# Performance work log

Measured on AMD Instinct MI355X. Metric: run time of the kernel, lower is better.

Reference implementation:

```python
import jax, jax.numpy as jnp
import numpy as np

EMBED_DIM = 1024
NUM_HEADS = 16
HEAD_DIM = EMBED_DIM // NUM_HEADS


def setup_inputs() -> dict:
    key = jax.random.key(0)
    ks = jax.random.split(key, 10)
    s = 1.0 / np.sqrt(EMBED_DIM)
    inp = {
        "x1": jax.random.normal(ks[0], (4, 1024, EMBED_DIM), jnp.float32),
        "x2": jax.random.normal(ks[1], (4, 2048, EMBED_DIM), jnp.float32),
        "Wq": jax.random.normal(ks[2], (EMBED_DIM, EMBED_DIM), jnp.float32) * s,
        "bq": jnp.zeros((EMBED_DIM,), jnp.float32),
        "Wk": jax.random.normal(ks[3], (EMBED_DIM, EMBED_DIM), jnp.float32) * s,
        "bk": jnp.zeros((EMBED_DIM,), jnp.float32),
        "Wv": jax.random.normal(ks[4], (EMBED_DIM, EMBED_DIM), jnp.float32) * s,
        "bv": jnp.zeros((EMBED_DIM,), jnp.float32),
        "Wo": jax.random.normal(ks[5], (EMBED_DIM, EMBED_DIM), jnp.float32) * s,
        "bo": jnp.zeros((EMBED_DIM,), jnp.float32),
    }
    return inp


def reference(x1, x2, Wq, bq, Wk, bk, Wv, bv, Wo, bo):
    B, Sq, E = x1.shape
    Skv = x2.shape[1]
    H, D = NUM_HEADS, HEAD_DIM
    # linear projections (PyTorch Linear: x @ W.T + b)
    q = (x1 @ Wq.T + bq).reshape(B, Sq, H, D).transpose(0, 2, 1, 3)   # [B,H,Sq,D]
    k = (x2 @ Wk.T + bk).reshape(B, Skv, H, D).transpose(0, 2, 1, 3)  # [B,H,Skv,D]
    v = (x2 @ Wv.T + bv).reshape(B, Skv, H, D).transpose(0, 2, 1, 3)
    scores = jnp.einsum("bhqd,bhkd->bhqk", q, k) / jnp.sqrt(jnp.float32(D))
    attn = jax.nn.softmax(scores, axis=-1)
    out = jnp.einsum("bhqk,bhkd->bhqd", attn, v)
    out = out.transpose(0, 2, 1, 3).reshape(B, Sq, E)
    return out @ Wo.T + bo
```

## Files before the change

### kernel.cpp

```cpp
#include <hip/hip_runtime.h>

typedef __attribute__((ext_vector_type(8))) short short8;
typedef __attribute__((ext_vector_type(4))) short short4v;
typedef __attribute__((ext_vector_type(4))) float f32x4;
typedef _Float16 half8 __attribute__((ext_vector_type(8)));

#define ASYNC16(g, l) __builtin_amdgcn_global_load_lds( \
    (__attribute__((address_space(1))) void*)(g), \
    (__attribute__((address_space(3))) void*)(l), 16, 0, 0)

__device__ __forceinline__ short f2bf(float f) {
  union { float f; unsigned u; } v; v.f = f;
  unsigned r = v.u + 0x7fffu + ((v.u >> 16) & 1u);
  return (short)(r >> 16);
}

__device__ __forceinline__ short f2h(float f) {
  _Float16 h = (_Float16)f;
  return __builtin_bit_cast(short, h);
}

__device__ __forceinline__ unsigned pkh2(float a, float b) {
  return __builtin_bit_cast(unsigned, __builtin_amdgcn_cvt_pkrtz(a, b));
}

__device__ __forceinline__ f32x4 fzero4() {
  f32x4 z; z[0] = 0.f; z[1] = 0.f; z[2] = 0.f; z[3] = 0.f; return z;
}

__device__ __forceinline__ void wg_barrier() {
  asm volatile("s_waitcnt lgkmcnt(0)\n\ts_barrier" ::: "memory");
}

__global__ __launch_bounds__(256) void cvt_all(
    const float* __restrict__ x1, const float* __restrict__ x2,
    const float* __restrict__ wq, const float* __restrict__ wk,
    const float* __restrict__ wv, const float* __restrict__ wo,
    short* __restrict__ dst) {
  long e = ((long)blockIdx.x * 256 + threadIdx.x) * 4;
  const float* src; long loc;
  if (e < 4194304L)       { src = x1; loc = e; }
  else if (e < 12582912L) { src = x2; loc = e - 4194304L; }
  else if (e < 13631488L) { src = wq; loc = e - 12582912L; }
  else if (e < 14680064L) { src = wk; loc = e - 13631488L; }
  else if (e < 15728640L) { src = wv; loc = e - 14680064L; }
  else                    { src = wo; loc = e - 15728640L; }
  float4 v = *(const float4*)(src + loc);
  short4v o;
  o[0] = f2bf(v.x); o[1] = f2bf(v.y); o[2] = f2bf(v.z); o[3] = f2bf(v.w);
  *(short4v*)(dst + e) = o;
}

__global__ __launch_bounds__(256) void proj(
    const short* __restrict__ xb1, const short* __restrict__ xb2,
    const short* __restrict__ wqp, const short* __restrict__ wkp, const short* __restrict__ wvp,
    const float* __restrict__ bq, const float* __restrict__ bk, const float* __restrict__ bv,
    short* __restrict__ qb, short* __restrict__ kb, short* __restrict__ vb) {
  __shared__ short smem[16384];
  short* As = smem;
  short* Bs = smem + 4096;
  const int tid = threadIdx.x, w = tid >> 6, lane = tid & 63;
  const int quad = lane >> 4, col = lane & 15;
  const int waveM = (w >> 1) * 64, waveN = (w & 1) * 64;
  const int my = blockIdx.x, bn = blockIdx.y * 128;
  const short* A; const short* W; const float* bias; int mode, bm;
  if (my < 32)      { A = xb1; W = wqp; bias = bq; mode = 0; bm = my * 128; }
  else if (my < 96) { A = xb2; W = wkp; bias = bk; mode = 1; bm = (my - 32) * 128; }
  else              { A = xb2; W = wvp; bias = bv; mode = 2; bm = (my - 96) * 128; }

  f32x4 acc[4][4];
  for (int mi = 0; mi < 4; ++mi)
    for (int ni = 0; ni < 4; ++ni)
      acc[mi][ni] = fzero4();

  const int srow = w * 16 + (lane >> 2), scol = (lane & 3) * 8;
  const short* ga = A + (size_t)(bm + srow) * 1024 + scol;
  const short* gb = W + (size_t)(bn + srow) * 1024 + scol;
  short* lA = As + w * 512;
  short* lB = Bs + w * 512;

  for (int kk = 0; kk < 1024; kk += 32) {
    __syncthreads();
    ASYNC16(ga + kk,         lA);
    ASYNC16(ga + kk + 65536, lA + 2048);
    ASYNC16(gb + kk,         lB);
    ASYNC16(gb + kk + 65536, lB + 2048);
    __syncthreads();
    short8 af[4], bf[4];
    for (int mi = 0; mi < 4; ++mi)
      af[mi] = *(const short8*)(As + (waveM + mi * 16 + col) * 32 + quad * 8);
    for (int ni = 0; ni < 4; ++ni)
      bf[ni] = *(const short8*)(Bs + (waveN + ni * 16 + col) * 32 + quad * 8);
    for (int mi = 0; mi < 4; ++mi)
      for (int ni = 0; ni < 4; ++ni)
        acc[mi][ni] = __builtin_amdgcn_mfma_f32_16x16x32_bf16(af[mi], bf[ni], acc[mi][ni], 0, 0, 0);
  }

  __syncthreads();
  for (int ni = 0; ni < 4; ++ni) {
    int nn = waveN + ni * 16 + col;
    float bvl = bias[bn + nn];
    for (int mi = 0; mi < 4; ++mi) {
      int m0 = waveM + mi * 16 + quad * 4;
      for (int r = 0; r < 4; ++r) {
        int m = m0 + r;
        float val = acc[mi][ni][r] + bvl;
        short sv;
        if (mode == 0)      sv = f2bf(val * 0.18033688011112042f);
        else if (mode == 1) sv = f2bf(val);
        else                sv = f2h(val);
        smem[m * 128 + (nn ^ ((m & 15) << 3))] = sv;
      }
    }
  }
  __syncthreads();
  if (mode < 2) {
    const int S = (mode == 0) ? 1024 : 2048;
    short* outp = (mode == 0) ? qb : kb;
    const int bb = bm / S, s0 = bm & (S - 1), h0 = bn >> 6;
    for (int it = 0; it < 8; ++it) {
      int f = (it * 256 + tid) * 8;
      int hh = f >> 13, rem = f & 8191, m = rem >> 6, d = rem & 63;
      int nn = hh * 64 + d;
      short8 val = *(const short8*)&smem[m * 128 + (nn ^ ((m & 15) << 3))];
      *(short8*)(outp + ((((size_t)(bb * 16 + h0 + hh)) * S + s0 + m) * 64 + d)) = val;
    }
  } else {
    const int bb = bm >> 11, s0 = bm & 2047, kt0 = s0 >> 6, h0 = bn >> 6;
    for (int it = 0; it < 8; ++it) {
      int f = (it * 256 + tid) * 8;
      int hh = f >> 13, rem = f & 8191, ktl = rem >> 12, r3 = rem & 4095;
      int d = r3 >> 6, kvp0 = r3 & 63;
      int nn = hh * 64 + d;
      short8 val;
      for (int j = 0; j < 8; ++j) {
        int kvp = kvp0 + j;
        int kv = ((kvp & 3) << 4) | (kvp >> 2);
        int m = ktl * 64 + kv;
        val[j] = smem[m * 128 + (nn ^ ((m & 15) << 3))];
      }
      *(short8*)(vb + ((((size_t)(bb * 16 + h0 + hh)) * 32 + (kt0 + ktl)) * 4096) + d * 64 + kvp0) = val;
    }
  }
}

__global__ __launch_bounds__(256) void out_gemm(
    const short* __restrict__ A, const short* __restrict__ W,
    const float* __restrict__ bias, float* __restrict__ out) {
  __shared__ short As[2][4096];
  __shared__ short Bs[2][2048];
  const int tid = threadIdx.x, w = tid >> 6, lane = tid & 63;
  const int quad = lane >> 4, col = lane & 15;
  const int waveM = (w >> 1) * 64, waveN = (w & 1) * 32;
  const int bn = blockIdx.x * 64, bm = blockIdx.y * 128;

  f32x4 acc[4][2];
  for (int mi = 0; mi < 4; ++mi)
    for (int ni = 0; ni < 2; ++ni)
      acc[mi][ni] = fzero4();

  const int arow = w * 16 + (lane >> 2), ac = (lane & 3) * 8;
  const short* ga = A + (size_t)(bm + arow) * 1024 + ac;
  const short* gb = W + (size_t)(bn + (tid >> 2)) * 1024 + (tid & 3) * 8;
  short* lA0 = As[0] + w * 512; short* lA1 = As[1] + w * 512;
  short* lB0 = Bs[0] + w * 512; short* lB1 = Bs[1] + w * 512;

  for (int kk = 0; kk < 1024; kk += 64) {
    __syncthreads();
    ASYNC16(ga + kk,              lA0);
    ASYNC16(ga + kk + 65536,      lA0 + 2048);
    ASYNC16(ga + kk + 32,         lA1);
    ASYNC16(ga + kk + 32 + 65536, lA1 + 2048);
    ASYNC16(gb + kk,              lB0);
    ASYNC16(gb + kk + 32,         lB1);
    __syncthreads();
    for (int kh = 0; kh < 2; ++kh) {
      const short* Ash = As[kh];
      const short* Bsh = Bs[kh];
      short8 af[4], bf[2];
      for (int mi = 0; mi < 4; ++mi)
        af[mi] = *(const short8*)(Ash + (waveM + mi * 16 + col) * 32 + quad * 8);
      for (int ni = 0; ni < 2; ++ni)
        bf[ni] = *(const short8*)(Bsh + (waveN + ni * 16 + col) * 32 + quad * 8);
      for (int mi = 0; mi < 4; ++mi)
        for (int ni = 0; ni < 2; ++ni)
          acc[mi][ni] = __builtin_amdgcn_mfma_f32_16x16x32_bf16(af[mi], bf[ni], acc[mi][ni], 0, 0, 0);
    }
  }

  for (int ni = 0; ni < 2; ++ni) {
    int n = bn + waveN + ni * 16 + col;
    float bvl = bias[n];
    for (int mi = 0; mi < 4; ++mi) {
      int m0 = bm + waveM + mi * 16 + quad * 4;
      for (int r = 0; r < 4; ++r)
        out[(size_t)(m0 + r) * 1024 + n] = acc[mi][ni][r] + bvl;
    }
  }
}

__global__ __launch_bounds__(256, 2) void attn(
    const short* __restrict__ Q, const short* __restrict__ K,
    const short* __restrict__ V, short* __restrict__ O) {
  __shared__ short Ks[128 * 72];
  __shared__ short Vs[80 * 136];
  __shared__ short Ps[128 * 136];
  const int tid = threadIdx.x, w = tid >> 6, lane = tid & 63;
  const int quad = lane >> 4, col = lane & 15;
  const int bh = blockIdx.x, qt = blockIdx.y;
  const int b = bh >> 4, h = bh & 15;
  const int qbase = w * 32;

  const short* qp = Q + ((size_t)bh * 1024 + qt * 128) * 64;
  const short* kp = K + (size_t)bh * 131072;
  const short* vp = V + (size_t)bh * 131072;

  short8 aq[2][2];
  for (int mi = 0; mi < 2; ++mi) {
    const short* qr = qp + (qbase + mi * 16 + col) * 64 + quad * 8;
    aq[mi][0] = *(const short8*)qr;
    aq[mi][1] = *(const short8*)(qr + 32);
  }

  f32x4 oa[2][5];
  for (int mi = 0; mi < 2; ++mi)
    for (int ni = 0; ni < 5; ++ni)
      oa[mi][ni] = fzero4();

  for (int i = tid; i < 16 * 136; i += 256)
    Vs[64 * 136 + i] = (i < 136) ? (short)0x3C00 : (short)0;

  const int krow = lane + (w >> 1) * 64, kch = (w & 1) * 32;
  const int vd = lane, vch = w & 1, vkh = (w >> 1) * 32;

  short8 kpre[4], vpre[4];
  {
    const short* kg = kp + krow * 64 + kch;
    const short* vg = vp + vch * 4096 + vd * 64 + vkh;
    for (int i = 0; i < 4; ++i) kpre[i] = *(const short8*)(kg + i * 8);
    for (int i = 0; i < 4; ++i) vpre[i] = *(const short8*)(vg + i * 8);
  }

  for (int kt = 0; kt < 16; ++kt) {
    wg_barrier();
    for (int i = 0; i < 4; ++i)
      *(short8*)&Ks[krow * 72 + kch + i * 8] = kpre[i];
    for (int i = 0; i < 4; ++i)
      *(short8*)&Vs[vd * 136 + vch * 64 + vkh + i * 8] = vpre[i];
    {
      int ktn = (kt < 15) ? kt + 1 : kt;
      const short* kg = kp + ktn * 8192 + krow * 64 + kch;
      const short* vg = vp + (2 * ktn + vch) * 4096 + vd * 64 + vkh;
      for (int i = 0; i < 4; ++i) kpre[i] = *(const short8*)(kg + i * 8);
      for (int i = 0; i < 4; ++i) vpre[i] = *(const short8*)(vg + i * 8);
    }
    wg_barrier();

    f32x4 sf[2][8];
    for (int nk = 0; nk < 8; ++nk) {
      short8 bk0 = *(const short8*)&Ks[(nk * 16 + col) * 72 + quad * 8];
      short8 bk1 = *(const short8*)&Ks[(nk * 16 + col) * 72 + 32 + quad * 8];
      f32x4 z0 = fzero4(), z1 = fzero4();
      z0 = __builtin_amdgcn_mfma_f32_16x16x32_bf16(aq[0][0], bk0, z0, 0, 0, 0);
      z0 = __builtin_amdgcn_mfma_f32_16x16x32_bf16(aq[0][1], bk1, z0, 0, 0, 0);
      z1 = __builtin_amdgcn_mfma_f32_16x16x32_bf16(aq[1][0], bk0, z1, 0, 0, 0);
      z1 = __builtin_amdgcn_mfma_f32_16x16x32_bf16(aq[1][1], bk1, z1, 0, 0, 0);
      sf[0][nk] = z0;
      sf[1][nk] = z1;
    }

    for (int mi = 0; mi < 2; ++mi)
      for (int nk = 0; nk < 8; ++nk)
        for (int r = 0; r < 4; ++r)
          sf[mi][nk][r] = __builtin_amdgcn_exp2f(sf[mi][nk][r]);
    for (int mi = 0; mi < 2; ++mi)
      for (int r = 0; r < 4; ++r) {
        int row = qbase + mi * 16 + quad * 4 + r;
        uint2 d0, d1;
        d0.x = pkh2(sf[mi][0][r], sf[mi][1][r]);
        d0.y = pkh2(sf[mi][2][r], sf[mi][3][r]);
        d1.x = pkh2(sf[mi][4][r], sf[mi][5][r]);
        d1.y = pkh2(sf[mi][6][r], sf[mi][7][r]);
        *(uint2*)&Ps[row * 136 + col * 4]      = d0;
        *(uint2*)&Ps[row * 136 + 64 + col * 4] = d1;
      }

    for (int ks = 0; ks < 4; ++ks) {
      int koff = ks * 32 + quad * 8;
      half8 ap0 = *(const half8*)&Ps[(qbase + col) * 136 + koff];
      half8 ap1 = *(const half8*)&Ps[(qbase + 16 + col) * 136 + koff];
      for (int ni = 0; ni < 5; ++ni) {
        half8 bv = *(const half8*)&Vs[(ni * 16 + col) * 136 + koff];
        oa[0][ni] = __builtin_amdgcn_mfma_f32_16x16x32_f16(ap0, bv, oa[0][ni], 0, 0, 0);
        oa[1][ni] = __builtin_amdgcn_mfma_f32_16x16x32_f16(ap1, bv, oa[1][ni], 0, 0, 0);
      }
    }
  }

  float inv[2][4];
  for (int mi = 0; mi < 2; ++mi)
    for (int r = 0; r < 4; ++r) {
      float s = __shfl(oa[mi][4][r], lane & 48);
      inv[mi][r] = 1.f / s;
    }
  __syncthreads();
  for (int mi = 0; mi < 2; ++mi)
    for (int ni = 0; ni < 4; ++ni)
      for (int r = 0; r < 4; ++r)
        Ps[(qbase + mi * 16 + quad * 4 + r) * 64 + ni * 16 + col] = f2bf(oa[mi][ni][r] * inv[mi][r]);
  __syncthreads();
  for (int it = 0; it < 4; ++it) {
    int f = (it * 256 + tid) * 8;
    int q = f >> 6, d = f & 63;
    short8 val = *(const short8*)&Ps[q * 64 + d];
    *(short8*)(O + ((size_t)(b * 1024 + qt * 128 + q)) * 1024 + h * 64 + d) = val;
  }
}

extern "C" void kernel_launch(void* const* d_in, const int* in_sizes, int n_in,
                              void* d_out, int out_size, void* d_ws, size_t ws_size,
                              hipStream_t stream) {
  const float* x1 = (const float*)d_in[0];
  const float* x2 = (const float*)d_in[1];
  const float* Wq = (const float*)d_in[2];
  const float* bq = (const float*)d_in[3];
  const float* Wk = (const float*)d_in[4];
  const float* bk = (const float*)d_in[5];
  const float* Wv = (const float*)d_in[6];
  const float* bv = (const float*)d_in[7];
  const float* Wo = (const float*)d_in[8];
  const float* bo = (const float*)d_in[9];

  char* ws = (char*)d_ws;
  short* xb1 = (short*)(ws + 0);
  short* xb2 = (short*)(ws + 8388608);
  short* wqb = (short*)(ws + 25165824);
  short* wkb = (short*)(ws + 27262976);
  short* wvb = (short*)(ws + 29360128);
  short* wob = (short*)(ws + 31457280);
  short* qb  = (short*)(ws + 33554432);
  short* kb  = (short*)(ws + 41943040);
  short* vb  = (short*)(ws + 58720256);
  short* ob  = (short*)(ws + 75497472);

  cvt_all<<<16384, 256, 0, stream>>>(x1, x2, Wq, Wk, Wv, Wo, (short*)ws);
  proj<<<dim3(160, 8), 256, 0, stream>>>(xb1, xb2, wqb, wkb, wvb, bq, bk, bv, qb, kb, vb);
  attn<<<dim3(64, 8), 256, 0, stream>>>(qb, kb, vb, ob);
  out_gemm<<<dim3(16, 32), 256, 0, stream>>>(ob, wob, bo, (float*)d_out);
}
```

Measured before the change: 240.6 us.

## Double K-step in projection GEMM and enlarge attention query tile to 256 rows

```diff
diff --git a/kernel.cpp b/kernel.cpp
--- a/kernel.cpp
+++ b/kernel.cpp
@@ -57,8 +57,6 @@
     const float* __restrict__ bq, const float* __restrict__ bk, const float* __restrict__ bv,
     short* __restrict__ qb, short* __restrict__ kb, short* __restrict__ vb) {
   __shared__ short smem[16384];
-  short* As = smem;
-  short* Bs = smem + 4096;
   const int tid = threadIdx.x, w = tid >> 6, lane = tid & 63;
   const int quad = lane >> 4, col = lane & 15;
   const int waveM = (w >> 1) * 64, waveN = (w & 1) * 64;
@@ -76,24 +74,34 @@
   const int srow = w * 16 + (lane >> 2), scol = (lane & 3) * 8;
   const short* ga = A + (size_t)(bm + srow) * 1024 + scol;
   const short* gb = W + (size_t)(bn + srow) * 1024 + scol;
-  short* lA = As + w * 512;
-  short* lB = Bs + w * 512;
-
-  for (int kk = 0; kk < 1024; kk += 32) {
+  short* lA0 = smem + w * 512;
+  short* lB0 = smem + 4096 + w * 512;
+  short* lA1 = smem + 8192 + w * 512;
+  short* lB1 = smem + 12288 + w * 512;
+
+  for (int kk = 0; kk < 1024; kk += 64) {
     __syncthreads();
-    ASYNC16(ga + kk,         lA);
-    ASYNC16(ga + kk + 65536, lA + 2048);
-    ASYNC16(gb + kk,         lB);
-    ASYNC16(gb + kk + 65536, lB + 2048);
+    ASYNC16(ga + kk,              lA0);
+    ASYNC16(ga + kk + 65536,      lA0 + 2048);
+    ASYNC16(gb + kk,              lB0);
+    ASYNC16(gb + kk + 65536,      lB0 + 2048);
+    ASYNC16(ga + kk + 32,         lA1);
+    ASYNC16(ga + kk + 32 + 65536, lA1 + 2048);
+    ASYNC16(gb + kk + 32,         lB1);
+    ASYNC16(gb + kk + 32 + 65536, lB1 + 2048);
     __syncthreads();
-    short8 af[4], bf[4];
-    for (int mi = 0; mi < 4; ++mi)
-      af[mi] = *(const short8*)(As + (waveM + mi * 16 + col) * 32 + quad * 8);
-    for (int ni = 0; ni < 4; ++ni)
-      bf[ni] = *(const short8*)(Bs + (waveN + ni * 16 + col) * 32 + quad * 8);
-    for (int mi = 0; mi < 4; ++mi)
+    for (int kh = 0; kh < 2; ++kh) {
+      const short* As = smem + kh * 8192;
+      const short* Bs = smem + 4096 + kh * 8192;
+      short8 af[4], bf[4];
+      for (int mi = 0; mi < 4; ++mi)
+        af[mi] = *(const short8*)(As + (waveM + mi * 16 + col) * 32 + quad * 8);
       for (int ni = 0; ni < 4; ++ni)
-        acc[mi][ni] = __builtin_amdgcn_mfma_f32_16x16x32_bf16(af[mi], bf[ni], acc[mi][ni], 0, 0, 0);
+        bf[ni] = *(const short8*)(Bs + (waveN + ni * 16 + col) * 32 + quad * 8);
+      for (int mi = 0; mi < 4; ++mi)
+        for (int ni = 0; ni < 4; ++ni)
+          acc[mi][ni] = __builtin_amdgcn_mfma_f32_16x16x32_bf16(af[mi], bf[ni], acc[mi][ni], 0, 0, 0);
+    }
   }
 
   __syncthreads();
@@ -199,36 +207,36 @@
   }
 }
 
-__global__ __launch_bounds__(256, 2) void attn(
+__global__ __launch_bounds__(256, 1) void attn(
     const short* __restrict__ Q, const short* __restrict__ K,
     const short* __restrict__ V, short* __restrict__ O) {
-  __shared__ short Ks[128 * 72];
-  __shared__ short Vs[80 * 136];
-  __shared__ short Ps[128 * 136];
+  __shared__ short Ks[128 * 74];
+  __shared__ short Vs[80 * 138];
+  __shared__ short Ps[256 * 138];
   const int tid = threadIdx.x, w = tid >> 6, lane = tid & 63;
   const int quad = lane >> 4, col = lane & 15;
   const int bh = blockIdx.x, qt = blockIdx.y;
   const int b = bh >> 4, h = bh & 15;
-  const int qbase = w * 32;
-
-  const short* qp = Q + ((size_t)bh * 1024 + qt * 128) * 64;
+  const int qbase = w * 64;
+
+  const short* qp = Q + ((size_t)bh * 1024 + qt * 256) * 64;
   const short* kp = K + (size_t)bh * 131072;
   const short* vp = V + (size_t)bh * 131072;
 
-  short8 aq[2][2];
-  for (int mi = 0; mi < 2; ++mi) {
+  short8 aq[4][2];
+  for (int mi = 0; mi < 4; ++mi) {
     const short* qr = qp + (qbase + mi * 16 + col) * 64 + quad * 8;
     aq[mi][0] = *(const short8*)qr;
     aq[mi][1] = *(const short8*)(qr + 32);
   }
 
-  f32x4 oa[2][5];
-  for (int mi = 0; mi < 2; ++mi)
+  f32x4 oa[4][5];
+  for (int mi = 0; mi < 4; ++mi)
     for (int ni = 0; ni < 5; ++ni)
       oa[mi][ni] = fzero4();
 
-  for (int i = tid; i < 16 * 136; i += 256)
-    Vs[64 * 136 + i] = (i < 136) ? (short)0x3C00 : (short)0;
+  for (int i = tid; i < 16 * 138; i += 256)
+    Vs[64 * 138 + i] = (i < 138) ? (short)0x3C00 : (short)0;
 
   const int krow = lane + (w >> 1) * 64, kch = (w & 1) * 32;
   const int vd = lane, vch = w & 1, vkh = (w >> 1) * 32;
@@ -244,9 +252,9 @@
   for (int kt = 0; kt < 16; ++kt) {
     wg_barrier();
     for (int i = 0; i < 4; ++i)
-      *(short8*)&Ks[krow * 72 + kch + i * 8] = kpre[i];
+      *(short8*)&Ks[krow * 74 + kch + i * 8] = kpre[i];
     for (int i = 0; i < 4; ++i)
-      *(short8*)&Vs[vd * 136 + vch * 64 + vkh + i * 8] = vpre[i];
+      *(short8*)&Vs[vd * 138 + vch * 64 + vkh + i * 8] = vpre[i];
     {
       int ktn = (kt < 15) ? kt + 1 : kt;
       const short* kg = kp + ktn * 8192 + krow * 64 + kch;
@@ -256,64 +264,64 @@
     }
     wg_barrier();
 
-    f32x4 sf[2][8];
-    for (int nk = 0; nk < 8; ++nk) {
-      short8 bk0 = *(const short8*)&Ks[(nk * 16 + col) * 72 + quad * 8];
-      short8 bk1 = *(const short8*)&Ks[(nk * 16 + col) * 72 + 32 + quad * 8];
-      f32x4 z0 = fzero4(), z1 = fzero4();
-      z0 = __builtin_amdgcn_mfma_f32_16x16x32_bf16(aq[0][0], bk0, z0, 0, 0, 0);
-      z0 = __builtin_amdgcn_mfma_f32_16x16x32_bf16(aq[0][1], bk1, z0, 0, 0, 0);
-      z1 = __builtin_amdgcn_mfma_f32_16x16x32_bf16(aq[1][0], bk0, z1, 0, 0, 0);
-      z1 = __builtin_amdgcn_mfma_f32_16x16x32_bf16(aq[1][1], bk1, z1, 0, 0, 0);
-      sf[0][nk] = z0;
-      sf[1][nk] = z1;
-    }
-
-    for (int mi = 0; mi < 2; ++mi)
-      for (int nk = 0; nk < 8; ++nk)
-        for (int r = 0; r < 4; ++r)
-          sf[mi][nk][r] = __builtin_amdgcn_exp2f(sf[mi][nk][r]);
-    for (int mi = 0; mi < 2; ++mi)
-      for (int r = 0; r < 4; ++r) {
-        int row = qbase + mi * 16 + quad * 4 + r;
-        uint2 d0, d1;
-        d0.x = pkh2(sf[mi][0][r], sf[mi][1][r]);
-        d0.y = pkh2(sf[mi][2][r], sf[mi][3][r]);
-        d1.x = pkh2(sf[mi][4][r], sf[mi][5][r]);
-        d1.y = pkh2(sf[mi][6][r], sf[mi][7][r]);
-        *(uint2*)&Ps[row * 136 + col * 4]      = d0;
-        *(uint2*)&Ps[row * 136 + 64 + col * 4] = d1;
-      }
+    for (int h2 = 0; h2 < 2; ++h2) {
+      short8 bk[4][2];
+      for (int nk = 0; nk < 4; ++nk) {
+        const short* kr = &Ks[((h2 * 4 + nk) * 16 + col) * 74 + quad * 8];
+        bk[nk][0] = *(const short8*)kr;
+        bk[nk][1] = *(const short8*)(kr + 32);
+      }
+      for (int mi = 0; mi < 4; ++mi) {
+        f32x4 sf[4];
+        for (int nk = 0; nk < 4; ++nk) {
+          f32x4 z = fzero4();
+          z = __builtin_amdgcn_mfma_f32_16x16x32_bf16(aq[mi][0], bk[nk][0], z, 0, 0, 0);
+          z = __builtin_amdgcn_mfma_f32_16x16x32_bf16(aq[mi][1], bk[nk][1], z, 0, 0, 0);
+          sf[nk] = z;
+        }
+        for (int nk = 0; nk < 4; ++nk)
+          for (int r = 0; r < 4; ++r)
+            sf[nk][r] = __builtin_amdgcn_exp2f(sf[nk][r]);
+        for (int r = 0; r < 4; ++r) {
+          int row = qbase + mi * 16 + quad * 4 + r;
+          uint2 d;
+          d.x = pkh2(sf[0][r], sf[1][r]);
+          d.y = pkh2(sf[2][r], sf[3][r]);
+          *(uint2*)&Ps[row * 138 + h2 * 64 + col * 4] = d;
+        }
+      }
+    }
 
     for (int ks = 0; ks < 4; ++ks) {
       int koff = ks * 32 + quad * 8;
-      half8 ap0 = *(const half8*)&Ps[(qbase + col) * 136 + koff];
-      half8 ap1 = *(const half8*)&Ps[(qbase + 16 + col) * 136 + koff];
-      for (int ni = 0; ni < 5; ++ni) {
-        half8 bv = *(const half8*)&Vs[(ni * 16 + col) * 136 + koff];
-        oa[0][ni] = __builtin_amdgcn_mfma_f32_16x16x32_f16(ap0, bv, oa[0][ni], 0, 0, 0);
-        oa[1][ni] = __builtin_amdgcn_mfma_f32_16x16x32_f16(ap1, bv, oa[1][ni], 0, 0, 0);
-      }
-    }
-  }
-
-  float inv[2][4];
-  for (int mi = 0; mi < 2; ++mi)
+      half8 bv[5];
+      for (int ni = 0; ni < 5; ++ni)
+        bv[ni] = *(const half8*)&Vs[(ni * 16 + col) * 138 + koff];
+      for (int mi = 0; mi < 4; ++mi) {
+        half8 ap = *(const half8*)&Ps[(qbase + mi * 16 + col) * 138 + koff];
+        for (int ni = 0; ni < 5; ++ni)
+          oa[mi][ni] = __builtin_amdgcn_mfma_f32_16x16x32_f16(ap, bv[ni], oa[mi][ni], 0, 0, 0);
+      }
+    }
+  }
+
+  float inv[4][4];
+  for (int mi = 0; mi < 4; ++mi)
     for (int r = 0; r < 4; ++r) {
       float s = __shfl(oa[mi][4][r], lane & 48);
       inv[mi][r] = 1.f / s;
     }
   __syncthreads();
-  for (int mi = 0; mi < 2; ++mi)
+  for (int mi = 0; mi < 4; ++mi)
     for (int ni = 0; ni < 4; ++ni)
       for (int r = 0; r < 4; ++r)
-        Ps[(qbase + mi * 16 + quad * 4 + r) * 64 + ni * 16 + col] = f2bf(oa[mi][ni][r] * inv[mi][r]);
+        Ps[(qbase + mi * 16 + quad * 4 + r) * 72 + ni * 16 + col] = f2bf(oa[mi][ni][r] * inv[mi][r]);
   __syncthreads();
-  for (int it = 0; it < 4; ++it) {
+  for (int it = 0; it < 8; ++it) {
     int f = (it * 256 + tid) * 8;
     int q = f >> 6, d = f & 63;
-    short8 val = *(const short8*)&Ps[q * 64 + d];
-    *(short8*)(O + ((size_t)(b * 1024 + qt * 128 + q)) * 1024 + h * 64 + d) = val;
+    short8 val = *(const short8*)&Ps[q * 72 + d];
+    *(short8*)(O + ((size_t)(b * 1024 + qt * 256 + q)) * 1024 + h * 64 + d) = val;
   }
 }
 
@@ -345,6 +353,6 @@
 
   cvt_all<<<16384, 256, 0, stream>>>(x1, x2, Wq, Wk, Wv, Wo, (short*)ws);
   proj<<<dim3(160, 8), 256, 0, stream>>>(xb1, xb2, wqb, wkb, wvb, bq, bk, bv, qb, kb, vb);
-  attn<<<dim3(64, 8), 256, 0, stream>>>(qb, kb, vb, ob);
+  attn<<<dim3(64, 4), 256, 0, stream>>>(qb, kb, vb, ob);
   out_gemm<<<dim3(16, 32), 256, 0, stream>>>(ob, wob, bo, (float*)d_out);
 }
```

After: 281.1 us. 1.17x slower.

## Double K-step in projection GEMM, retile V layout, and repad attention LDS

Applied to the files above, without the earlier changes.

```diff
diff --git a/kernel.cpp b/kernel.cpp
--- a/kernel.cpp
+++ b/kernel.cpp
@@ -57,8 +57,6 @@
     const float* __restrict__ bq, const float* __restrict__ bk, const float* __restrict__ bv,
     short* __restrict__ qb, short* __restrict__ kb, short* __restrict__ vb) {
   __shared__ short smem[16384];
-  short* As = smem;
-  short* Bs = smem + 4096;
   const int tid = threadIdx.x, w = tid >> 6, lane = tid & 63;
   const int quad = lane >> 4, col = lane & 15;
   const int waveM = (w >> 1) * 64, waveN = (w & 1) * 64;
@@ -76,24 +74,34 @@
   const int srow = w * 16 + (lane >> 2), scol = (lane & 3) * 8;
   const short* ga = A + (size_t)(bm + srow) * 1024 + scol;
   const short* gb = W + (size_t)(bn + srow) * 1024 + scol;
-  short* lA = As + w * 512;
-  short* lB = Bs + w * 512;
-
-  for (int kk = 0; kk < 1024; kk += 32) {
+  short* lA0 = smem + w * 512;
+  short* lB0 = smem + 4096 + w * 512;
+  short* lA1 = smem + 8192 + w * 512;
+  short* lB1 = smem + 12288 + w * 512;
+
+  for (int kk = 0; kk < 1024; kk += 64) {
     __syncthreads();
-    ASYNC16(ga + kk,         lA);
-    ASYNC16(ga + kk + 65536, lA + 2048);
-    ASYNC16(gb + kk,         lB);
-    ASYNC16(gb + kk + 65536, lB + 2048);
+    ASYNC16(ga + kk,              lA0);
+    ASYNC16(ga + kk + 65536,      lA0 + 2048);
+    ASYNC16(gb + kk,              lB0);
+    ASYNC16(gb + kk + 65536,      lB0 + 2048);
+    ASYNC16(ga + kk + 32,         lA1);
+    ASYNC16(ga + kk + 32 + 65536, lA1 + 2048);
+    ASYNC16(gb + kk + 32,         lB1);
+    ASYNC16(gb + kk + 32 + 65536, lB1 + 2048);
     __syncthreads();
-    short8 af[4], bf[4];
-    for (int mi = 0; mi < 4; ++mi)
-      af[mi] = *(const short8*)(As + (waveM + mi * 16 + col) * 32 + quad * 8);
-    for (int ni = 0; ni < 4; ++ni)
-      bf[ni] = *(const short8*)(Bs + (waveN + ni * 16 + col) * 32 + quad * 8);
-    for (int mi = 0; mi < 4; ++mi)
+    for (int kh = 0; kh < 2; ++kh) {
+      const short* As = smem + kh * 8192;
+      const short* Bs = smem + 4096 + kh * 8192;
+      short8 af[4], bf[4];
+      for (int mi = 0; mi < 4; ++mi)
+        af[mi] = *(const short8*)(As + (waveM + mi * 16 + col) * 32 + quad * 8);
       for (int ni = 0; ni < 4; ++ni)
-        acc[mi][ni] = __builtin_amdgcn_mfma_f32_16x16x32_bf16(af[mi], bf[ni], acc[mi][ni], 0, 0, 0);
+        bf[ni] = *(const short8*)(Bs + (waveN + ni * 16 + col) * 32 + quad * 8);
+      for (int mi = 0; mi < 4; ++mi)
+        for (int ni = 0; ni < 4; ++ni)
+          acc[mi][ni] = __builtin_amdgcn_mfma_f32_16x16x32_bf16(af[mi], bf[ni], acc[mi][ni], 0, 0, 0);
+    }
   }
 
   __syncthreads();
@@ -126,20 +134,18 @@
       *(short8*)(outp + ((((size_t)(bb * 16 + h0 + hh)) * S + s0 + m) * 64 + d)) = val;
     }
   } else {
-    const int bb = bm >> 11, s0 = bm & 2047, kt0 = s0 >> 6, h0 = bn >> 6;
+    const int bb = bm >> 11, s0 = bm & 2047, kt = s0 >> 7, h0 = bn >> 6;
     for (int it = 0; it < 8; ++it) {
       int f = (it * 256 + tid) * 8;
-      int hh = f >> 13, rem = f & 8191, ktl = rem >> 12, r3 = rem & 4095;
-      int d = r3 >> 6, kvp0 = r3 & 63;
+      int hh = f >> 13, rem = f & 8191, d = rem >> 7, kq0 = rem & 127;
       int nn = hh * 64 + d;
       short8 val;
       for (int j = 0; j < 8; ++j) {
-        int kvp = kvp0 + j;
-        int kv = ((kvp & 3) << 4) | (kvp >> 2);
-        int m = ktl * 64 + kv;
+        int kvpp = kq0 + j;
+        int m = ((kvpp & 7) << 4) | (kvpp >> 3);
         val[j] = smem[m * 128 + (nn ^ ((m & 15) << 3))];
       }
-      *(short8*)(vb + ((((size_t)(bb * 16 + h0 + hh)) * 32 + (kt0 + ktl)) * 4096) + d * 64 + kvp0) = val;
+      *(short8*)(vb + ((((size_t)(bb * 16 + h0 + hh)) * 16 + kt) * 8192) + d * 128 + kq0) = val;
     }
   }
 }
@@ -202,9 +208,9 @@
 __global__ __launch_bounds__(256, 2) void attn(
     const short* __restrict__ Q, const short* __restrict__ K,
     const short* __restrict__ V, short* __restrict__ O) {
-  __shared__ short Ks[128 * 72];
-  __shared__ short Vs[80 * 136];
-  __shared__ short Ps[128 * 136];
+  __shared__ short Ks[128 * 74];
+  __shared__ short Vs[80 * 138];
+  __shared__ short Ps[128 * 138];
   const int tid = threadIdx.x, w = tid >> 6, lane = tid & 63;
   const int quad = lane >> 4, col = lane & 15;
   const int bh = blockIdx.x, qt = blockIdx.y;
@@ -227,16 +233,16 @@
     for (int ni = 0; ni < 5; ++ni)
       oa[mi][ni] = fzero4();
 
-  for (int i = tid; i < 16 * 136; i += 256)
-    Vs[64 * 136 + i] = (i < 136) ? (short)0x3C00 : (short)0;
+  for (int i = tid; i < 16 * 138; i += 256)
+    Vs[64 * 138 + i] = (i < 138) ? (short)0x3C00 : (short)0;
 
   const int krow = lane + (w >> 1) * 64, kch = (w & 1) * 32;
-  const int vd = lane, vch = w & 1, vkh = (w >> 1) * 32;
+  const int vd = lane, vq = w * 32;
 
   short8 kpre[4], vpre[4];
   {
     const short* kg = kp + krow * 64 + kch;
-    const short* vg = vp + vch * 4096 + vd * 64 + vkh;
+    const short* vg = vp + vd * 128 + vq;
     for (int i = 0; i < 4; ++i) kpre[i] = *(const short8*)(kg + i * 8);
     for (int i = 0; i < 4; ++i) vpre[i] = *(const short8*)(vg + i * 8);
   }
@@ -244,13 +250,13 @@
   for (int kt = 0; kt < 16; ++kt) {
     wg_barrier();
     for (int i = 0; i < 4; ++i)
-      *(short8*)&Ks[krow * 72 + kch + i * 8] = kpre[i];
+      *(short8*)&Ks[krow * 74 + kch + i * 8] = kpre[i];
     for (int i = 0; i < 4; ++i)
-      *(short8*)&Vs[vd * 136 + vch * 64 + vkh + i * 8] = vpre[i];
+      *(short8*)&Vs[vd * 138 + vq + i * 8] = vpre[i];
     {
       int ktn = (kt < 15) ? kt + 1 : kt;
       const short* kg = kp + ktn * 8192 + krow * 64 + kch;
-      const short* vg = vp + (2 * ktn + vch) * 4096 + vd * 64 + vkh;
+      const short* vg = vp + ktn * 8192 + vd * 128 + vq;
       for (int i = 0; i < 4; ++i) kpre[i] = *(const short8*)(kg + i * 8);
       for (int i = 0; i < 4; ++i) vpre[i] = *(const short8*)(vg + i * 8);
     }
@@ -258,8 +264,8 @@
 
     f32x4 sf[2][8];
     for (int nk = 0; nk < 8; ++nk) {
-      short8 bk0 = *(const short8*)&Ks[(nk * 16 + col) * 72 + quad * 8];
-      short8 bk1 = *(const short8*)&Ks[(nk * 16 + col) * 72 + 32 + quad * 8];
+      short8 bk0 = *(const short8*)&Ks[(nk * 16 + col) * 74 + quad * 8];
+      short8 bk1 = *(const short8*)&Ks[(nk * 16 + col) * 74 + 32 + quad * 8];
       f32x4 z0 = fzero4(), z1 = fzero4();
       z0 = __builtin_amdgcn_mfma_f32_16x16x32_bf16(aq[0][0], bk0, z0, 0, 0, 0);
       z0 = __builtin_amdgcn_mfma_f32_16x16x32_bf16(aq[0][1], bk1, z0, 0, 0, 0);
@@ -276,21 +282,20 @@
     for (int mi = 0; mi < 2; ++mi)
       for (int r = 0; r < 4; ++r) {
         int row = qbase + mi * 16 + quad * 4 + r;
-        uint2 d0, d1;
-        d0.x = pkh2(sf[mi][0][r], sf[mi][1][r]);
-        d0.y = pkh2(sf[mi][2][r], sf[mi][3][r]);
-        d1.x = pkh2(sf[mi][4][r], sf[mi][5][r]);
-        d1.y = pkh2(sf[mi][6][r], sf[mi][7][r]);
-        *(uint2*)&Ps[row * 136 + col * 4]      = d0;
-        *(uint2*)&Ps[row * 136 + 64 + col * 4] = d1;
+        uint4 d;
+        d.x = pkh2(sf[mi][0][r], sf[mi][1][r]);
+        d.y = pkh2(sf[mi][2][r], sf[mi][3][r]);
+        d.z = pkh2(sf[mi][4][r], sf[mi][5][r]);
+        d.w = pkh2(sf[mi][6][r], sf[mi][7][r]);
+        *(uint4*)&Ps[row * 138 + col * 8] = d;
       }
 
     for (int ks = 0; ks < 4; ++ks) {
       int koff = ks * 32 + quad * 8;
-      half8 ap0 = *(const half8*)&Ps[(qbase + col) * 136 + koff];
-      half8 ap1 = *(const half8*)&Ps[(qbase + 16 + col) * 136 + koff];
+      half8 ap0 = *(const half8*)&Ps[(qbase + col) * 138 + koff];
+      half8 ap1 = *(const half8*)&Ps[(qbase + 16 + col) * 138 + koff];
       for (int ni = 0; ni < 5; ++ni) {
-        half8 bv = *(const half8*)&Vs[(ni * 16 + col) * 136 + koff];
+        half8 bv = *(const half8*)&Vs[(ni * 16 + col) * 138 + koff];
         oa[0][ni] = __builtin_amdgcn_mfma_f32_16x16x32_f16(ap0, bv, oa[0][ni], 0, 0, 0);
         oa[1][ni] = __builtin_amdgcn_mfma_f32_16x16x32_f16(ap1, bv, oa[1][ni], 0, 0, 0);
       }
@@ -307,12 +312,12 @@
   for (int mi = 0; mi < 2; ++mi)
     for (int ni = 0; ni < 4; ++ni)
       for (int r = 0; r < 4; ++r)
-        Ps[(qbase + mi * 16 + quad * 4 + r) * 64 + ni * 16 + col] = f2bf(oa[mi][ni][r] * inv[mi][r]);
+        Ps[(qbase + mi * 16 + quad * 4 + r) * 72 + ni * 16 + col] = f2bf(oa[mi][ni][r] * inv[mi][r]);
   __syncthreads();
   for (int it = 0; it < 4; ++it) {
     int f = (it * 256 + tid) * 8;
     int q = f >> 6, d = f & 63;
-    short8 val = *(const short8*)&Ps[q * 64 + d];
+    short8 val = *(const short8*)&Ps[q * 72 + d];
     *(short8*)(O + ((size_t)(b * 1024 + qt * 128 + q)) * 1024 + h * 64 + d) = val;
   }
 }
```

After: 267.9 us. 1.11x slower.
